# Kernel optimization log

Hardware: AMD Instinct MI355X
Metric: run time of the kernel (lower is better)

## Reference

```python
import jax, jax.numpy as jnp
import numpy as np

B, L = 8, 2048
AMP, ANG = 48, 16
H = 4
AQK, GQK = 12, 6   # amp/ang qk head dims
AV, GV = 12, 6     # amp/ang v head dims
LOOKBACK = 100


def setup_inputs() -> dict:
    key = jax.random.key(0)
    ks = jax.random.split(key, 16)
    def w(k, i, o):
        # kaiming-uniform-ish scale; stored [in, out] so forward is x @ W
        bound = 1.0 / np.sqrt(i)
        return jax.random.uniform(k, (i, o), jnp.float32, -bound, bound)
    return dict(
        x_ang=jax.random.normal(ks[0], (B, L, 2 * ANG), jnp.float32),
        x_amp=jax.random.normal(ks[1], (B, L, AMP), jnp.float32),
        Wq_amp=w(ks[2], AMP, H * AQK),
        Wk_amp=w(ks[3], AMP, H * AQK),
        Wv_amp=w(ks[4], AMP, H * AV),
        Wq_ang_r=w(ks[5], ANG, H * GQK),
        Wq_ang_i=w(ks[6], ANG, H * GQK),
        Wk_ang_r=w(ks[7], ANG, H * GQK),
        Wk_ang_i=w(ks[8], ANG, H * GQK),
        Wv_ang_r=w(ks[9], ANG, H * GV),
        Wv_ang_i=w(ks[10], ANG, H * GV),
        Wout_amp=w(ks[11], H * AV, AMP),
        bout_amp=jax.random.uniform(ks[12], (AMP,), jnp.float32, -0.1, 0.1),
        Wout_ang_r=w(ks[13], H * GV, ANG),
        Wout_ang_i=w(ks[14], H * GV, ANG),
    )


def _clin(xr, xi, Wr, Wi):
    # complex linear: (xr + i xi) @ (Wr + i Wi)
    return xr @ Wr - xi @ Wi, xr @ Wi + xi @ Wr


def reference(x_ang, x_amp, Wq_amp, Wk_amp, Wv_amp,
              Wq_ang_r, Wq_ang_i, Wk_ang_r, Wk_ang_i,
              Wv_ang_r, Wv_ang_i, Wout_amp, bout_amp,
              Wout_ang_r, Wout_ang_i):
    Bb, Ll, CA = x_ang.shape
    ang_r, ang_i = jnp.split(x_ang, 2, axis=-1)

    def heads(x, hd):  # [B,L,H*hd] -> [B,H,L,hd]
        return x.reshape(Bb, Ll, H, hd).transpose(0, 2, 1, 3)

    q_amp = heads(x_amp @ Wq_amp, AQK)
    k_amp = heads(x_amp @ Wk_amp, AQK)
    qar, qai = _clin(ang_r, ang_i, Wq_ang_r, Wq_ang_i)
    kar, kai = _clin(ang_r, ang_i, Wk_ang_r, Wk_ang_i)
    q = jnp.concatenate([heads(qar, GQK), heads(qai, GQK), q_amp], axis=-1)  # [B,H,L,24]
    k = jnp.concatenate([heads(kar, GQK), heads(kai, GQK), k_amp], axis=-1)

    v_amp = heads(x_amp @ Wv_amp, AV)
    var, vai = _clin(ang_r, ang_i, Wv_ang_r, Wv_ang_i)
    v = jnp.concatenate([heads(var, GV), heads(vai, GV), v_amp], axis=-1)  # [B,H,L,24]

    scale = 1.0 / jnp.sqrt(jnp.asarray(q.shape[-1], q.dtype))
    scores = jnp.einsum('bhqd,bhkd->bhqk', q, k) * scale
    idx = jnp.arange(Ll)
    valid = (idx[None, :] <= idx[:, None]) & (idx[None, :] >= idx[:, None] - (LOOKBACK - 1))
    mask = jnp.where(valid, jnp.asarray(0.0, scores.dtype), jnp.finfo(scores.dtype).min)
    attn = jax.nn.softmax(scores + mask, axis=-1)
    out = jnp.einsum('bhqk,bhkd->bhqd', attn, v)  # [B,H,L,24]

    o_ang_r, o_ang_i, o_amp = jnp.split(out, [GV, 2 * GV], axis=-1)

    def merge(x):  # [B,H,L,hd] -> [B,L,H*hd]
        return x.transpose(0, 2, 1, 3).reshape(Bb, Ll, -1)

    out_amp = merge(o_amp) @ Wout_amp + bout_amp
    out_ang_r, out_ang_i = _clin(merge(o_ang_r), merge(o_ang_i), Wout_ang_r, Wout_ang_i)
    return (out_ang_r, out_ang_i, out_amp)
```

## Files before the change

kernel.cpp:

```cpp
#include <hip/hip_runtime.h>
#include <hip/hip_bf16.h>

constexpr int B = 8;
constexpr int L = 2048;
constexpr int ANG = 16;
constexpr int AMP = 48;
constexpr int H = 4;
constexpr int AQK = 12, GQK = 6;
constexpr int AV = 12, GV = 6;
constexpr int HD = 2 * GQK + AQK;
constexpr int LOOKBACK = 100;

constexpr int NTOK = B * L;

constexpr int QKV_AMP_JOBS = NTOK * 48;
constexpr int QKV_ANG_JOBS = NTOK * 72;
constexpr int QKV_AMP_BLOCKS = QKV_AMP_JOBS / 256;
constexpr int QKV_ANG_BLOCKS = QKV_ANG_JOBS / 256;

__global__ __launch_bounds__(256) void qkv2_kernel(
    const float* __restrict__ x_ang, const float* __restrict__ x_amp,
    const float* __restrict__ Wq_amp, const float* __restrict__ Wk_amp,
    const float* __restrict__ Wv_amp,
    const float* __restrict__ Wq_ang_r, const float* __restrict__ Wq_ang_i,
    const float* __restrict__ Wk_ang_r, const float* __restrict__ Wk_ang_i,
    const float* __restrict__ Wv_ang_r, const float* __restrict__ Wv_ang_i,
    float* __restrict__ q, float* __restrict__ k, float* __restrict__ v)
{
    int bid = blockIdx.x;
    if (bid < QKV_AMP_BLOCKS) {
        int g   = bid * 256 + threadIdx.x;
        int col = g % 48;
        int tok = g / 48;

        const float4* xm4 = (const float4*)(x_amp + (size_t)tok * AMP);
        float x[48];
        #pragma unroll
        for (int i = 0; i < 12; i++) {
            float4 t = xm4[i];
            x[4*i+0] = t.x; x[4*i+1] = t.y; x[4*i+2] = t.z; x[4*i+3] = t.w;
        }

        float aq = 0.f, ak = 0.f, av = 0.f;
        #pragma unroll
        for (int i = 0; i < 48; i++) {
            aq += x[i] * Wq_amp[i * 48 + col];
            ak += x[i] * Wk_amp[i * 48 + col];
            av += x[i] * Wv_amp[i * 48 + col];
        }

        int b = tok / L, l = tok % L;
        int h = col / 12, ca = col % 12;
        size_t o = (((size_t)b * H + h) * L + l) * HD + (2 * GQK) + ca;
        q[o] = aq; k[o] = ak; v[o] = av;
    } else {
        int g     = (bid - QKV_AMP_BLOCKS) * 256 + threadIdx.x;
        int j     = g % 72;
        int tok   = g / 72;
        int mat   = j / 24;
        int combo = j % 24;
        int h     = combo / 6, dd = combo % 6;

        const float4* xa4 = (const float4*)(x_ang + (size_t)tok * (2 * ANG));
        float xr[16], xi[16];
        #pragma unroll
        for (int i = 0; i < 4; i++) {
            float4 t = xa4[i];
            xr[4*i+0] = t.x; xr[4*i+1] = t.y; xr[4*i+2] = t.z; xr[4*i+3] = t.w;
            float4 u = xa4[4 + i];
            xi[4*i+0] = u.x; xi[4*i+1] = u.y; xi[4*i+2] = u.z; xi[4*i+3] = u.w;
        }

        const float* Wr = (mat == 0) ? Wq_ang_r : (mat == 1) ? Wk_ang_r : Wv_ang_r;
        const float* Wi = (mat == 0) ? Wq_ang_i : (mat == 1) ? Wk_ang_i : Wv_ang_i;

        float orr = 0.f, oii = 0.f;
        #pragma unroll
        for (int i = 0; i < 16; i++) {
            float wr = Wr[i * 24 + combo], wi = Wi[i * 24 + combo];
            orr += xr[i] * wr - xi[i] * wi;
            oii += xr[i] * wi + xi[i] * wr;
        }

        float* dst = (mat == 0) ? q : (mat == 1) ? k : v;
        int b = tok / L, l = tok % L;
        size_t base = (((size_t)b * H + h) * L + l) * HD;
        dst[base + dd]       = orr;
        dst[base + GQK + dd] = oii;
    }
}

constexpr int TQA    = 64;
constexpr int GROUPS = 4;
constexpr int MAXKA  = TQA + LOOKBACK - 1;

__global__ __launch_bounds__(256) void attn3_kernel(
    const float* __restrict__ q, const float* __restrict__ k,
    const float* __restrict__ v, float* __restrict__ att)
{
    constexpr int NT = L / TQA;
    int bh = blockIdx.x / NT;
    int qt = blockIdx.x % NT;
    int q0 = qt * TQA;
    int kmin = q0 - (LOOKBACK - 1); if (kmin < 0) kmin = 0;
    int nrows = (q0 + TQA - 1) - kmin + 1;

    __shared__ float4 Ks4[MAXKA][8];
    __shared__ float4 Vs4[MAXKA][8];
    __shared__ float  Pm[GROUPS][TQA];
    __shared__ float  Ps[GROUPS][TQA];
    __shared__ float4 Po4[GROUPS][TQA][6];

    {
        const float4* kb4 = (const float4*)(k + ((size_t)bh * L + kmin) * HD);
        const float4* vb4 = (const float4*)(v + ((size_t)bh * L + kmin) * HD);
        int nch = nrows * 6;
        for (int c = threadIdx.x; c < nch; c += 256) {
            int r = c / 6, s = c % 6;
            int slot = s ^ (r & 7);
            Ks4[r][slot] = kb4[c];
            Vs4[r][slot] = vb4[c];
        }
    }
    __syncthreads();

    int qlocal = threadIdx.x & (TQA - 1);
    int group  = threadIdx.x >> 6;
    int qi = q0 + qlocal;

    float4 qr4[6];
    {
        const float4* qp4 = (const float4*)(q + ((size_t)bh * L + qi) * HD);
        #pragma unroll
        for (int s = 0; s < 6; s++) qr4[s] = qp4[s];
    }

    const float scale = 0.2041241452319315f;
    float m = -3.0e38f, ss = 0.f;
    float4 o4[6];
    #pragma unroll
    for (int s = 0; s < 6; s++) { o4[s].x = 0.f; o4[s].y = 0.f; o4[s].z = 0.f; o4[s].w = 0.f; }

    int j0 = qi - (LOOKBACK - 1); if (j0 < 0) j0 = 0;
    for (int j = j0 + group; j <= qi; j += GROUPS) {
        int r  = j - kmin;
        int rx = r & 7;
        float sc = 0.f;
        #pragma unroll
        for (int s = 0; s < 6; s++) {
            float4 kk = Ks4[r][s ^ rx];
            sc += qr4[s].x * kk.x + qr4[s].y * kk.y + qr4[s].z * kk.z + qr4[s].w * kk.w;
        }
        sc *= scale;
        float mn   = fmaxf(m, sc);
        float corr = __expf(m - mn);
        float p    = __expf(sc - mn);
        ss = ss * corr + p;
        #pragma unroll
        for (int s = 0; s < 6; s++) {
            float4 vv = Vs4[r][s ^ rx];
            o4[s].x = o4[s].x * corr + p * vv.x;
            o4[s].y = o4[s].y * corr + p * vv.y;
            o4[s].z = o4[s].z * corr + p * vv.z;
            o4[s].w = o4[s].w * corr + p * vv.w;
        }
        m = mn;
    }

    Pm[group][qlocal] = m;
    Ps[group][qlocal] = ss;
    #pragma unroll
    for (int s = 0; s < 6; s++) Po4[group][qlocal][s] = o4[s];
    __syncthreads();

    {
        int qq    = threadIdx.x & 63;
        int chunk = threadIdx.x >> 6;
        float m0 = Pm[0][qq], m1 = Pm[1][qq], m2 = Pm[2][qq], m3 = Pm[3][qq];
        float mm = fmaxf(fmaxf(m0, m1), fmaxf(m2, m3));
        float c0 = __expf(m0 - mm), c1 = __expf(m1 - mm);
        float c2 = __expf(m2 - mm), c3 = __expf(m3 - mm);
        float denom = Ps[0][qq] * c0 + Ps[1][qq] * c1 + Ps[2][qq] * c2 + Ps[3][qq] * c3;
        float inv = 1.f / denom;

        float4* op4 = (float4*)(att + ((size_t)bh * L + q0 + qq) * HD);

        int s = chunk;
        {
            float4 a0 = Po4[0][qq][s], a1 = Po4[1][qq][s], a2 = Po4[2][qq][s], a3 = Po4[3][qq][s];
            float4 acc;
            acc.x = (a0.x * c0 + a1.x * c1 + a2.x * c2 + a3.x * c3) * inv;
            acc.y = (a0.y * c0 + a1.y * c1 + a2.y * c2 + a3.y * c3) * inv;
            acc.z = (a0.z * c0 + a1.z * c1 + a2.z * c2 + a3.z * c3) * inv;
            acc.w = (a0.w * c0 + a1.w * c1 + a2.w * c2 + a3.w * c3) * inv;
            op4[s] = acc;
        }
        if (chunk < 2) {
            s = chunk + 4;
            float4 a0 = Po4[0][qq][s], a1 = Po4[1][qq][s], a2 = Po4[2][qq][s], a3 = Po4[3][qq][s];
            float4 acc;
            acc.x = (a0.x * c0 + a1.x * c1 + a2.x * c2 + a3.x * c3) * inv;
            acc.y = (a0.y * c0 + a1.y * c1 + a2.y * c2 + a3.y * c3) * inv;
            acc.z = (a0.z * c0 + a1.z * c1 + a2.z * c2 + a3.z * c3) * inv;
            acc.w = (a0.w * c0 + a1.w * c1 + a2.w * c2 + a3.w * c3) * inv;
            op4[s] = acc;
        }
    }
}

constexpr int PAMP_JOBS   = NTOK * 48;
constexpr int PANG_JOBS   = NTOK * 16;
constexpr int PAMP_BLOCKS = PAMP_JOBS / 256;
constexpr int PANG_BLOCKS = PANG_JOBS / 256;

__global__ __launch_bounds__(256) void proj2_kernel(
    const float* __restrict__ att,
    const float* __restrict__ Wout_amp, const float* __restrict__ bout_amp,
    const float* __restrict__ Wout_ang_r, const float* __restrict__ Wout_ang_i,
    float* __restrict__ out)
{
    constexpr size_t ANG_OUT = (size_t)NTOK * ANG;
    int bid = blockIdx.x;

    if (bid < PAMP_BLOCKS) {
        int g   = bid * 256 + threadIdx.x;
        int col = g % 48;
        int tok = g / 48;
        int b = tok / L, l = tok % L;

        float a[48];
        #pragma unroll
        for (int h = 0; h < H; h++) {
            const float4* ap4 = (const float4*)(att + (((size_t)b * H + h) * L + l) * HD + 2 * GV);
            #pragma unroll
            for (int i = 0; i < 3; i++) {
                float4 t = ap4[i];
                a[h*12 + 4*i+0] = t.x; a[h*12 + 4*i+1] = t.y;
                a[h*12 + 4*i+2] = t.z; a[h*12 + 4*i+3] = t.w;
            }
        }
        float acc = bout_amp[col];
        #pragma unroll
        for (int i = 0; i < 48; i++)
            acc += a[i] * Wout_amp[i * AMP + col];
        out[2 * ANG_OUT + (size_t)tok * AMP + col] = acc;
    } else {
        int g   = (bid - PAMP_BLOCKS) * 256 + threadIdx.x;
        int col = g % 16;
        int tok = g / 16;
        int b = tok / L, l = tok % L;

        float ar[24], ai[24];
        #pragma unroll
        for (int h = 0; h < H; h++) {
            const float4* ap4 = (const float4*)(att + (((size_t)b * H + h) * L + l) * HD);
            float4 t0 = ap4[0], t1 = ap4[1], t2 = ap4[2];
            ar[h*6+0] = t0.x; ar[h*6+1] = t0.y; ar[h*6+2] = t0.z; ar[h*6+3] = t0.w;
            ar[h*6+4] = t1.x; ar[h*6+5] = t1.y;
            ai[h*6+0] = t1.z; ai[h*6+1] = t1.w;
            ai[h*6+2] = t2.x; ai[h*6+3] = t2.y; ai[h*6+4] = t2.z; ai[h*6+5] = t2.w;
        }
        float accr = 0.f, acci = 0.f;
        #pragma unroll
        for (int i = 0; i < 24; i++) {
            float wr = Wout_ang_r[i * ANG + col], wi = Wout_ang_i[i * ANG + col];
            accr += ar[i] * wr - ai[i] * wi;
            acci += ar[i] * wi + ai[i] * wr;
        }
        out[(size_t)tok * ANG + col]           = accr;
        out[ANG_OUT + (size_t)tok * ANG + col] = acci;
    }
}

extern "C" void kernel_launch(void* const* d_in, const int* in_sizes, int n_in,
                              void* d_out, int out_size, void* d_ws, size_t ws_size,
                              hipStream_t stream)
{
    const float* x_ang      = (const float*)d_in[0];
    const float* x_amp      = (const float*)d_in[1];
    const float* Wq_amp     = (const float*)d_in[2];
    const float* Wk_amp     = (const float*)d_in[3];
    const float* Wv_amp     = (const float*)d_in[4];
    const float* Wq_ang_r   = (const float*)d_in[5];
    const float* Wq_ang_i   = (const float*)d_in[6];
    const float* Wk_ang_r   = (const float*)d_in[7];
    const float* Wk_ang_i   = (const float*)d_in[8];
    const float* Wv_ang_r   = (const float*)d_in[9];
    const float* Wv_ang_i   = (const float*)d_in[10];
    const float* Wout_amp   = (const float*)d_in[11];
    const float* bout_amp   = (const float*)d_in[12];
    const float* Wout_ang_r = (const float*)d_in[13];
    const float* Wout_ang_i = (const float*)d_in[14];

    float* out = (float*)d_out;
    float* ws  = (float*)d_ws;

    const size_t N = (size_t)B * H * L * HD;
    float* q   = ws;
    float* k   = ws + N;
    float* v   = ws + 2 * N;
    float* att = ws + 3 * N;

    qkv2_kernel<<<QKV_AMP_BLOCKS + QKV_ANG_BLOCKS, 256, 0, stream>>>(
        x_ang, x_amp, Wq_amp, Wk_amp, Wv_amp,
        Wq_ang_r, Wq_ang_i, Wk_ang_r, Wk_ang_i, Wv_ang_r, Wv_ang_i,
        q, k, v);

    attn3_kernel<<<B * H * (L / TQA), 256, 0, stream>>>(q, k, v, att);

    proj2_kernel<<<PAMP_BLOCKS + PANG_BLOCKS, 256, 0, stream>>>(
        att, Wout_amp, bout_amp, Wout_ang_r, Wout_ang_i, out);
}
```

Baseline: 154.5 us.

## Fuse QKV projection into attention kernel and store attention output token-major

Removes the separate QKV projection kernel. Each attention block now stages its window of raw x_amp/x_ang rows in shared memory and computes K/V for the 163-row halo plus Q for its 64 queries in registers, then writes them into shared tiles through a union that reuses the staging memory. The q/k/v global round trip goes away, at the cost of recomputing K/V for overlapping lookback rows, about 1.5x redundant work. The attention output layout becomes [B,L,H,24] so the projection kernel reads each token contiguously. There are leftover dead pointer computations in the store code.

```diff
diff --git a/kernel.cpp b/kernel.cpp
--- a/kernel.cpp
+++ b/kernel.cpp
@@ -10,136 +10,185 @@
 constexpr int AV = 12, GV = 6;
 constexpr int HD = 2 * GQK + AQK;
 constexpr int LOOKBACK = 100;
-
 constexpr int NTOK = B * L;
 
-constexpr int QKV_AMP_JOBS = NTOK * 48;
-constexpr int QKV_ANG_JOBS = NTOK * 72;
-constexpr int QKV_AMP_BLOCKS = QKV_AMP_JOBS / 256;
-constexpr int QKV_ANG_BLOCKS = QKV_ANG_JOBS / 256;
-
-__global__ __launch_bounds__(256) void qkv2_kernel(
+constexpr int TQ     = 64;
+constexpr int GROUPS = 4;
+constexpr int MAXK   = TQ + LOOKBACK - 1;
+constexpr int NT     = L / TQ;
+
+struct StageT {
+    float xam[MAXK][49];
+    float xan[MAXK][33];
+};
+struct TileT {
+    float4 Ks[MAXK][8];
+    float4 Vs[MAXK][8];
+    float4 Qs[TQ][6];
+};
+union SharedU { StageT stage; TileT t; };
+
+__global__ __launch_bounds__(256) void fused_qkv_attn_kernel(
     const float* __restrict__ x_ang, const float* __restrict__ x_amp,
     const float* __restrict__ Wq_amp, const float* __restrict__ Wk_amp,
     const float* __restrict__ Wv_amp,
     const float* __restrict__ Wq_ang_r, const float* __restrict__ Wq_ang_i,
     const float* __restrict__ Wk_ang_r, const float* __restrict__ Wk_ang_i,
     const float* __restrict__ Wv_ang_r, const float* __restrict__ Wv_ang_i,
-    float* __restrict__ q, float* __restrict__ k, float* __restrict__ v)
+    float* __restrict__ att)
 {
-    int bid = blockIdx.x;
-    if (bid < QKV_AMP_BLOCKS) {
-        int g   = bid * 256 + threadIdx.x;
-        int col = g % 48;
-        int tok = g / 48;
-
-        const float4* xm4 = (const float4*)(x_amp + (size_t)tok * AMP);
-        float x[48];
-        #pragma unroll
-        for (int i = 0; i < 12; i++) {
-            float4 t = xm4[i];
-            x[4*i+0] = t.x; x[4*i+1] = t.y; x[4*i+2] = t.z; x[4*i+3] = t.w;
-        }
-
-        float aq = 0.f, ak = 0.f, av = 0.f;
-        #pragma unroll
-        for (int i = 0; i < 48; i++) {
-            aq += x[i] * Wq_amp[i * 48 + col];
-            ak += x[i] * Wk_amp[i * 48 + col];
-            av += x[i] * Wv_amp[i * 48 + col];
-        }
-
-        int b = tok / L, l = tok % L;
-        int h = col / 12, ca = col % 12;
-        size_t o = (((size_t)b * H + h) * L + l) * HD + (2 * GQK) + ca;
-        q[o] = aq; k[o] = ak; v[o] = av;
-    } else {
-        int g     = (bid - QKV_AMP_BLOCKS) * 256 + threadIdx.x;
-        int j     = g % 72;
-        int tok   = g / 72;
-        int mat   = j / 24;
-        int combo = j % 24;
-        int h     = combo / 6, dd = combo % 6;
-
-        const float4* xa4 = (const float4*)(x_ang + (size_t)tok * (2 * ANG));
-        float xr[16], xi[16];
-        #pragma unroll
-        for (int i = 0; i < 4; i++) {
-            float4 t = xa4[i];
-            xr[4*i+0] = t.x; xr[4*i+1] = t.y; xr[4*i+2] = t.z; xr[4*i+3] = t.w;
-            float4 u = xa4[4 + i];
-            xi[4*i+0] = u.x; xi[4*i+1] = u.y; xi[4*i+2] = u.z; xi[4*i+3] = u.w;
-        }
-
-        const float* Wr = (mat == 0) ? Wq_ang_r : (mat == 1) ? Wk_ang_r : Wv_ang_r;
-        const float* Wi = (mat == 0) ? Wq_ang_i : (mat == 1) ? Wk_ang_i : Wv_ang_i;
-
-        float orr = 0.f, oii = 0.f;
-        #pragma unroll
-        for (int i = 0; i < 16; i++) {
-            float wr = Wr[i * 24 + combo], wi = Wi[i * 24 + combo];
-            orr += xr[i] * wr - xi[i] * wi;
-            oii += xr[i] * wi + xi[i] * wr;
-        }
-
-        float* dst = (mat == 0) ? q : (mat == 1) ? k : v;
-        int b = tok / L, l = tok % L;
-        size_t base = (((size_t)b * H + h) * L + l) * HD;
-        dst[base + dd]       = orr;
-        dst[base + GQK + dd] = oii;
-    }
-}
-
-constexpr int TQA    = 64;
-constexpr int GROUPS = 4;
-constexpr int MAXKA  = TQA + LOOKBACK - 1;
-
-__global__ __launch_bounds__(256) void attn3_kernel(
-    const float* __restrict__ q, const float* __restrict__ k,
-    const float* __restrict__ v, float* __restrict__ att)
-{
-    constexpr int NT = L / TQA;
-    int bh = blockIdx.x / NT;
-    int qt = blockIdx.x % NT;
-    int q0 = qt * TQA;
+    __shared__ SharedU u;
+    __shared__ float  Pm[GROUPS][TQ];
+    __shared__ float  Ps[GROUPS][TQ];
+    __shared__ float4 Po[GROUPS][TQ][6];
+
+    const int tid = threadIdx.x;
+    const int bh  = blockIdx.x / NT;
+    const int qt  = blockIdx.x % NT;
+    const int b   = bh / H, h = bh % H;
+    const int q0  = qt * TQ;
     int kmin = q0 - (LOOKBACK - 1); if (kmin < 0) kmin = 0;
-    int nrows = (q0 + TQA - 1) - kmin + 1;
-
-    __shared__ float4 Ks4[MAXKA][8];
-    __shared__ float4 Vs4[MAXKA][8];
-    __shared__ float  Pm[GROUPS][TQA];
-    __shared__ float  Ps[GROUPS][TQA];
-    __shared__ float4 Po4[GROUPS][TQA][6];
+    const int nrows = (q0 + TQ - 1) - kmin + 1;
+    const int qoff  = q0 - kmin;
 
     {
-        const float4* kb4 = (const float4*)(k + ((size_t)bh * L + kmin) * HD);
-        const float4* vb4 = (const float4*)(v + ((size_t)bh * L + kmin) * HD);
-        int nch = nrows * 6;
-        for (int c = threadIdx.x; c < nch; c += 256) {
-            int r = c / 6, s = c % 6;
-            int slot = s ^ (r & 7);
-            Ks4[r][slot] = kb4[c];
-            Vs4[r][slot] = vb4[c];
+        const float4* xm4 = (const float4*)(x_amp + ((size_t)b * L + kmin) * AMP);
+        const float4* xg4 = (const float4*)(x_ang + ((size_t)b * L + kmin) * (2 * ANG));
+        int namp = nrows * 12;
+        int ntot = namp + nrows * 8;
+        for (int c = tid; c < ntot; c += 256) {
+            if (c < namp) {
+                int r = c / 12, i = c % 12;
+                float4 t = xm4[c];
+                float* p = &u.stage.xam[r][4 * i];
+                p[0] = t.x; p[1] = t.y; p[2] = t.z; p[3] = t.w;
+            } else {
+                int c2 = c - namp;
+                int r = c2 / 8, i = c2 % 8;
+                float4 t = xg4[c2];
+                float* p = &u.stage.xan[r][4 * i];
+                p[0] = t.x; p[1] = t.y; p[2] = t.z; p[3] = t.w;
+            }
         }
     }
     __syncthreads();
 
-    int qlocal = threadIdx.x & (TQA - 1);
-    int group  = threadIdx.x >> 6;
-    int qi = q0 + qlocal;
+    float4 kout[6], vout[6], qout[6];
+    const bool kvact = (tid < nrows);
+    const bool qact  = (tid >= 192);
+    const int  qrow  = tid - 192;
+
+    #pragma unroll
+    for (int s = 0; s < 6; ++s) {
+        if (kvact) {
+            int r = tid;
+            if (s >= 3) {
+                int col4 = h * AQK + (s - 3) * 4;
+                const float* Wk = Wk_amp + col4;
+                const float* Wv = Wv_amp + col4;
+                float4 ka = {0,0,0,0}, va = {0,0,0,0};
+                #pragma unroll
+                for (int i = 0; i < AMP; ++i) {
+                    float x = u.stage.xam[r][i];
+                    float4 wk = *(const float4*)(Wk + i * 48);
+                    float4 wv = *(const float4*)(Wv + i * 48);
+                    ka.x += x * wk.x; ka.y += x * wk.y; ka.z += x * wk.z; ka.w += x * wk.w;
+                    va.x += x * wv.x; va.y += x * wv.y; va.z += x * wv.z; va.w += x * wv.w;
+                }
+                kout[s] = ka; vout[s] = va;
+            } else {
+                float kk[4], vv[4];
+                #pragma unroll
+                for (int c = 0; c < 4; ++c) {
+                    int d = 4 * s + c;
+                    bool re = (d < GQK);
+                    int dd = re ? d : d - GQK;
+                    int col = h * GQK + dd;
+                    const float* WkA = re ? Wk_ang_r : Wk_ang_i;
+                    const float* WkB = re ? Wk_ang_i : Wk_ang_r;
+                    const float* WvA = re ? Wv_ang_r : Wv_ang_i;
+                    const float* WvB = re ? Wv_ang_i : Wv_ang_r;
+                    float sgn = re ? -1.f : 1.f;
+                    float ak = 0, bk = 0, aw = 0, bw = 0;
+                    #pragma unroll
+                    for (int i = 0; i < ANG; ++i) {
+                        float xr = u.stage.xan[r][i];
+                        float xi = u.stage.xan[r][16 + i];
+                        ak += xr * WkA[i * 24 + col];  bk += xi * WkB[i * 24 + col];
+                        aw += xr * WvA[i * 24 + col];  bw += xi * WvB[i * 24 + col];
+                    }
+                    kk[c] = ak + sgn * bk;  vv[c] = aw + sgn * bw;
+                }
+                kout[s] = make_float4(kk[0], kk[1], kk[2], kk[3]);
+                vout[s] = make_float4(vv[0], vv[1], vv[2], vv[3]);
+            }
+        }
+        if (qact) {
+            int r = qoff + qrow;
+            if (s >= 3) {
+                int col4 = h * AQK + (s - 3) * 4;
+                const float* Wq = Wq_amp + col4;
+                float4 qa = {0,0,0,0};
+                #pragma unroll
+                for (int i = 0; i < AMP; ++i) {
+                    float x = u.stage.xam[r][i];
+                    float4 wq = *(const float4*)(Wq + i * 48);
+                    qa.x += x * wq.x; qa.y += x * wq.y; qa.z += x * wq.z; qa.w += x * wq.w;
+                }
+                qout[s] = qa;
+            } else {
+                float qq[4];
+                #pragma unroll
+                for (int c = 0; c < 4; ++c) {
+                    int d = 4 * s + c;
+                    bool re = (d < GQK);
+                    int dd = re ? d : d - GQK;
+                    int col = h * GQK + dd;
+                    const float* WA = re ? Wq_ang_r : Wq_ang_i;
+                    const float* WB = re ? Wq_ang_i : Wq_ang_r;
+                    float sgn = re ? -1.f : 1.f;
+                    float aa = 0, bb = 0;
+                    #pragma unroll
+                    for (int i = 0; i < ANG; ++i) {
+                        float xr = u.stage.xan[r][i];
+                        float xi = u.stage.xan[r][16 + i];
+                        aa += xr * WA[i * 24 + col];  bb += xi * WB[i * 24 + col];
+                    }
+                    qq[c] = aa + sgn * bb;
+                }
+                qout[s] = make_float4(qq[0], qq[1], qq[2], qq[3]);
+            }
+        }
+    }
+    __syncthreads();
+
+    if (kvact) {
+        int r = tid, rx = r & 7;
+        #pragma unroll
+        for (int s = 0; s < 6; ++s) {
+            u.t.Ks[r][s ^ rx] = kout[s];
+            u.t.Vs[r][s ^ rx] = vout[s];
+        }
+    }
+    if (qact) {
+        #pragma unroll
+        for (int s = 0; s < 6; ++s) u.t.Qs[qrow][s] = qout[s];
+    }
+    __syncthreads();
+
+    const int qlocal = tid & (TQ - 1);
+    const int group  = tid >> 6;
+    const int qi = q0 + qlocal;
 
     float4 qr4[6];
-    {
-        const float4* qp4 = (const float4*)(q + ((size_t)bh * L + qi) * HD);
-        #pragma unroll
-        for (int s = 0; s < 6; s++) qr4[s] = qp4[s];
-    }
+    #pragma unroll
+    for (int s = 0; s < 6; ++s) qr4[s] = u.t.Qs[qlocal][s];
 
     const float scale = 0.2041241452319315f;
     float m = -3.0e38f, ss = 0.f;
     float4 o4[6];
     #pragma unroll
-    for (int s = 0; s < 6; s++) { o4[s].x = 0.f; o4[s].y = 0.f; o4[s].z = 0.f; o4[s].w = 0.f; }
+    for (int s = 0; s < 6; ++s) { o4[s].x = 0.f; o4[s].y = 0.f; o4[s].z = 0.f; o4[s].w = 0.f; }
 
     int j0 = qi - (LOOKBACK - 1); if (j0 < 0) j0 = 0;
     for (int j = j0 + group; j <= qi; j += GROUPS) {
@@ -147,8 +196,8 @@
         int rx = r & 7;
         float sc = 0.f;
         #pragma unroll
-        for (int s = 0; s < 6; s++) {
-            float4 kk = Ks4[r][s ^ rx];
+        for (int s = 0; s < 6; ++s) {
+            float4 kk = u.t.Ks[r][s ^ rx];
             sc += qr4[s].x * kk.x + qr4[s].y * kk.y + qr4[s].z * kk.z + qr4[s].w * kk.w;
         }
         sc *= scale;
@@ -157,8 +206,8 @@
         float p    = __expf(sc - mn);
         ss = ss * corr + p;
         #pragma unroll
-        for (int s = 0; s < 6; s++) {
-            float4 vv = Vs4[r][s ^ rx];
+        for (int s = 0; s < 6; ++s) {
+            float4 vv = u.t.Vs[r][s ^ rx];
             o4[s].x = o4[s].x * corr + p * vv.x;
             o4[s].y = o4[s].y * corr + p * vv.y;
             o4[s].z = o4[s].z * corr + p * vv.z;
@@ -170,12 +219,12 @@
     Pm[group][qlocal] = m;
     Ps[group][qlocal] = ss;
     #pragma unroll
-    for (int s = 0; s < 6; s++) Po4[group][qlocal][s] = o4[s];
+    for (int s = 0; s < 6; ++s) Po[group][qlocal][s] = o4[s];
     __syncthreads();
 
     {
-        int qq    = threadIdx.x & 63;
-        int chunk = threadIdx.x >> 6;
+        int qq    = tid & 63;
+        int chunk = tid >> 6;
         float m0 = Pm[0][qq], m1 = Pm[1][qq], m2 = Pm[2][qq], m3 = Pm[3][qq];
         float mm = fmaxf(fmaxf(m0, m1), fmaxf(m2, m3));
         float c0 = __expf(m0 - mm), c1 = __expf(m1 - mm);
@@ -183,37 +232,37 @@
         float denom = Ps[0][qq] * c0 + Ps[1][qq] * c1 + Ps[2][qq] * c2 + Ps[3][qq] * c3;
         float inv = 1.f / denom;
 
-        float4* op4 = (float4*)(att + ((size_t)bh * L + q0 + qq) * HD);
+        float4* op4 = (float4*)att + (size_t)(b * L + q0 + qq) * 6 * H / H * H;
+        op4 = (float4*)att + ((size_t)(b * L + q0 + qq) * H + h) * 0;
+        float4* dst = (float4*)att + (size_t)(b * L + q0 + qq) * 24 + h * 6;
 
         int s = chunk;
         {
-            float4 a0 = Po4[0][qq][s], a1 = Po4[1][qq][s], a2 = Po4[2][qq][s], a3 = Po4[3][qq][s];
+            float4 a0 = Po[0][qq][s], a1 = Po[1][qq][s], a2 = Po[2][qq][s], a3 = Po[3][qq][s];
             float4 acc;
             acc.x = (a0.x * c0 + a1.x * c1 + a2.x * c2 + a3.x * c3) * inv;
             acc.y = (a0.y * c0 + a1.y * c1 + a2.y * c2 + a3.y * c3) * inv;
             acc.z = (a0.z * c0 + a1.z * c1 + a2.z * c2 + a3.z * c3) * inv;
             acc.w = (a0.w * c0 + a1.w * c1 + a2.w * c2 + a3.w * c3) * inv;
-            op4[s] = acc;
+            dst[s] = acc;
         }
         if (chunk < 2) {
             s = chunk + 4;
-            float4 a0 = Po4[0][qq][s], a1 = Po4[1][qq][s], a2 = Po4[2][qq][s], a3 = Po4[3][qq][s];
+            float4 a0 = Po[0][qq][s], a1 = Po[1][qq][s], a2 = Po[2][qq][s], a3 = Po[3][qq][s];
             float4 acc;
             acc.x = (a0.x * c0 + a1.x * c1 + a2.x * c2 + a3.x * c3) * inv;
             acc.y = (a0.y * c0 + a1.y * c1 + a2.y * c2 + a3.y * c3) * inv;
             acc.z = (a0.z * c0 + a1.z * c1 + a2.z * c2 + a3.z * c3) * inv;
             acc.w = (a0.w * c0 + a1.w * c1 + a2.w * c2 + a3.w * c3) * inv;
-            op4[s] = acc;
+            dst[s] = acc;
         }
     }
 }
 
-constexpr int PAMP_JOBS   = NTOK * 48;
-constexpr int PANG_JOBS   = NTOK * 16;
-constexpr int PAMP_BLOCKS = PAMP_JOBS / 256;
-constexpr int PANG_BLOCKS = PANG_JOBS / 256;
-
-__global__ __launch_bounds__(256) void proj2_kernel(
+constexpr int PAMP_BLOCKS = (NTOK * 48) / 256;
+constexpr int PANG_BLOCKS = (NTOK * 16) / 256;
+
+__global__ __launch_bounds__(256) void proj3_kernel(
     const float* __restrict__ att,
     const float* __restrict__ Wout_amp, const float* __restrict__ bout_amp,
     const float* __restrict__ Wout_ang_r, const float* __restrict__ Wout_ang_i,
@@ -226,15 +275,14 @@
         int g   = bid * 256 + threadIdx.x;
         int col = g % 48;
         int tok = g / 48;
-        int b = tok / L, l = tok % L;
+        const float4* at4 = (const float4*)att + (size_t)tok * 24;
 
         float a[48];
         #pragma unroll
         for (int h = 0; h < H; h++) {
-            const float4* ap4 = (const float4*)(att + (((size_t)b * H + h) * L + l) * HD + 2 * GV);
             #pragma unroll
             for (int i = 0; i < 3; i++) {
-                float4 t = ap4[i];
+                float4 t = at4[h * 6 + 3 + i];
                 a[h*12 + 4*i+0] = t.x; a[h*12 + 4*i+1] = t.y;
                 a[h*12 + 4*i+2] = t.z; a[h*12 + 4*i+3] = t.w;
             }
@@ -248,13 +296,12 @@
         int g   = (bid - PAMP_BLOCKS) * 256 + threadIdx.x;
         int col = g % 16;
         int tok = g / 16;
-        int b = tok / L, l = tok % L;
+        const float4* at4 = (const float4*)att + (size_t)tok * 24;
 
         float ar[24], ai[24];
         #pragma unroll
         for (int h = 0; h < H; h++) {
-            const float4* ap4 = (const float4*)(att + (((size_t)b * H + h) * L + l) * HD);
-            float4 t0 = ap4[0], t1 = ap4[1], t2 = ap4[2];
+            float4 t0 = at4[h*6+0], t1 = at4[h*6+1], t2 = at4[h*6+2];
             ar[h*6+0] = t0.x; ar[h*6+1] = t0.y; ar[h*6+2] = t0.z; ar[h*6+3] = t0.w;
             ar[h*6+4] = t1.x; ar[h*6+5] = t1.y;
             ai[h*6+0] = t1.z; ai[h*6+1] = t1.w;
@@ -293,21 +340,13 @@
     const float* Wout_ang_i = (const float*)d_in[14];
 
     float* out = (float*)d_out;
-    float* ws  = (float*)d_ws;
-
-    const size_t N = (size_t)B * H * L * HD;
-    float* q   = ws;
-    float* k   = ws + N;
-    float* v   = ws + 2 * N;
-    float* att = ws + 3 * N;
-
-    qkv2_kernel<<<QKV_AMP_BLOCKS + QKV_ANG_BLOCKS, 256, 0, stream>>>(
+    float* att = (float*)d_ws;
+
+    fused_qkv_attn_kernel<<<B * H * NT, 256, 0, stream>>>(
         x_ang, x_amp, Wq_amp, Wk_amp, Wv_amp,
         Wq_ang_r, Wq_ang_i, Wk_ang_r, Wk_ang_i, Wv_ang_r, Wv_ang_i,
-        q, k, v);
-
-    attn3_kernel<<<B * H * (L / TQA), 256, 0, stream>>>(q, k, v, att);
-
-    proj2_kernel<<<PAMP_BLOCKS + PANG_BLOCKS, 256, 0, stream>>>(
+        att);
+
+    proj3_kernel<<<PAMP_BLOCKS + PANG_BLOCKS, 256, 0, stream>>>(
         att, Wout_amp, bout_amp, Wout_ang_r, Wout_ang_i, out);
 }
```

Measured after the change: 153.2 us. No clear change (-0.8%).
